# Performance work log

Hardware: AMD Instinct MI355X
Metric: run time of the kernel (lower is better)

## Reference

```python
import jax, jax.numpy as jnp
import numpy as np

OUT_H, OUT_W = 64, 64  # glimpse size (layer's output_dim)
B, IMG_H, IMG_W, CH = 32, 512, 512, 3


def setup_inputs() -> dict:
    key = jax.random.key(0)
    k_img, k_u, k_s, k_d, k_u2, k_s2, k_d2 = jax.random.split(key, 7)
    img_tensor = jax.random.uniform(k_img, (B, IMG_H, IMG_W, CH), dtype=jnp.float32)
    # DRAW-style params per sample: (uy, sy, dy, ux, sx, dx)
    # centres u in [0, img - glimpse], sigma s in [1, 5], stride d in [1, img/glimpse]
    uy = jax.random.uniform(k_u, (B, 1), minval=0.0, maxval=IMG_H - OUT_H * 2.0)
    sy = jax.random.uniform(k_s, (B, 1), minval=1.0, maxval=5.0)
    dy = jax.random.uniform(k_d, (B, 1), minval=1.0, maxval=IMG_H / OUT_H)
    ux = jax.random.uniform(k_u2, (B, 1), minval=0.0, maxval=IMG_W - OUT_W * 2.0)
    sx = jax.random.uniform(k_s2, (B, 1), minval=1.0, maxval=5.0)
    dx = jax.random.uniform(k_d2, (B, 1), minval=1.0, maxval=IMG_W / OUT_W)
    transform_params = jnp.concatenate([uy, sy, dy, ux, sx, dx], axis=-1)  # (B, 6)
    return {"img_tensor": img_tensor, "transform_params": transform_params}


def gaussian_mask(u, s, d, R, C):
    """Normalized Gaussian filterbank.
    u, s, d: (B, 1) centre of first Gaussian, std, stride between centres.
    R: number of glimpse rows/cols; C: image size along that axis.
    Returns (B, C, R), each column normalized to sum 1 (plus eps)."""
    r = jnp.arange(R, dtype=jnp.float32).reshape(1, 1, R)
    c = jnp.arange(C, dtype=jnp.float32).reshape(1, C, 1)
    centres = u[:, None, :] + r * d[:, None, :]            # (B, 1, R)
    mask = jnp.exp(-0.5 * jnp.square((c - centres) / s[:, None, :]))  # (B, C, R)
    return mask / (jnp.sum(mask, axis=1, keepdims=True) + 1e-8)


def reference(img_tensor, transform_params):
    # img_tensor: (B, h, w, ch); transform_params: (B, 6)
    _, h, w, _ = img_tensor.shape
    uy, sy, dy, ux, sx, dx = jnp.split(transform_params, 6, axis=-1)
    Ay = gaussian_mask(uy, sy, dy, OUT_H, h)  # (B, h, OUT_H)
    Ax = gaussian_mask(ux, sx, dx, OUT_W, w)  # (B, w, OUT_W)
    # glimpse = Ay^T @ img @ Ax, applied per channel
    g = jnp.einsum('bhH,bhwc->bHwc', Ay, img_tensor)   # (B, OUT_H, w, ch)
    return jnp.einsum('bHwc,bwW->bHWc', g, Ax)         # (B, OUT_H, OUT_W, ch)
```

## Files before the change

kernel.cpp:

```cpp
#include <hip/hip_runtime.h>
#include <stdint.h>

#define BATCH 32
#define IMG 512
#define CH 3
#define GOUT 64
#define ROWB (IMG*CH)
#define GP   ((size_t)BATCH*CH*GOUT*IMG)

typedef __attribute__((ext_vector_type(8))) short  short8;
typedef __attribute__((ext_vector_type(4))) float  floatx4;

__device__ __forceinline__ unsigned short f2bf(float x) {
    unsigned u = __builtin_bit_cast(unsigned, x);
    u += 0x7FFFu + ((u >> 16) & 1u);
    return (unsigned short)(u >> 16);
}

__global__ __launch_bounds__(64) void mask_kernel(const float* __restrict__ tp,
                                                  unsigned short* __restrict__ AyT,
                                                  unsigned short* __restrict__ AxT) {
    int blk  = blockIdx.x;
    int r    = blk & 63;
    int axis = (blk >> 6) & 1;
    int b    = blk >> 7;

    const float* p = tp + b*6 + (axis ? 3 : 0);
    float u = p[0], s = p[1], d = p[2];
    float centre = u + (float)r * d;
    float inv_s  = 1.0f / s;

    int lane = threadIdx.x;
    float e[8];
    float sum = 0.0f;
    #pragma unroll
    for (int i = 0; i < 8; ++i) {
        float z = ((float)(i*64 + lane) - centre) * inv_s;
        e[i] = __expf(-0.5f * z * z);
        sum += e[i];
    }
    #pragma unroll
    for (int m = 1; m < 64; m <<= 1)
        sum += __shfl_xor(sum, m, 64);
    float inv_sum = 1.0f / (sum + 1e-8f);

    unsigned short* dst = (axis ? AxT : AyT) + ((size_t)b*GOUT + r) * IMG;
    #pragma unroll
    for (int i = 0; i < 8; ++i)
        dst[i*64 + lane] = f2bf(e[i] * inv_sum);
}

__global__ __launch_bounds__(256, 4) void stage1_kernel(const float* __restrict__ img,
                                                        const unsigned short* __restrict__ AyT,
                                                        float* __restrict__ gP) {
    int part = blockIdx.x & 1;
    int bt   = blockIdx.x >> 1;
    int tile = bt % 24;
    int b    = bt / 24;
    int wc0  = tile * 64;
    int tid  = threadIdx.x;
    int wave = tid >> 6;
    int lane = tid & 63;
    int n16  = lane & 15;
    int q    = lane >> 4;

    floatx4 acc[4];
    #pragma unroll
    for (int mt = 0; mt < 4; ++mt) acc[mt] = (floatx4){0.f, 0.f, 0.f, 0.f};

    const float*          imb = img + (size_t)b * IMG * ROWB + wc0 + wave*16 + n16;
    const unsigned short* ayb = AyT + (size_t)b * GOUT * IMG;

    for (int h0 = part*256; h0 < part*256 + 256; h0 += 32) {
        int hk = h0 + q*8;
        const float* ip = imb + (size_t)hk * ROWB;
        short8 bf;
        #pragma unroll
        for (int j = 0; j < 8; ++j)
            bf[j] = (short)f2bf(ip[(size_t)j * ROWB]);
        #pragma unroll
        for (int mt = 0; mt < 4; ++mt) {
            short8 af = *(const short8*)(ayb + (size_t)(mt*16 + n16) * IMG + hk);
            acc[mt] = __builtin_amdgcn_mfma_f32_16x16x32_bf16(af, bf, acc[mt], 0, 0, 0);
        }
    }

    int wc = wc0 + wave*16 + n16;
    int c = wc % 3, w = wc / 3;
    float* gb = gP + (size_t)part * GP + ((size_t)(b*CH + c) * GOUT) * IMG + w;
    #pragma unroll
    for (int mt = 0; mt < 4; ++mt)
        #pragma unroll
        for (int reg = 0; reg < 4; ++reg)
            gb[(size_t)(mt*16 + q*4 + reg) * IMG] = acc[mt][reg];
}

__global__ __launch_bounds__(256) void stage2_kernel(const float* __restrict__ gP,
                                                     const unsigned short* __restrict__ AxT,
                                                     float* __restrict__ out) {
    int blk  = blockIdx.x;
    int hq   = blk & 3;
    int bc   = blk >> 2;
    int c    = bc % 3;
    int b    = bc / 3;
    int tid  = threadIdx.x;
    int wave = tid >> 6;
    int lane = tid & 63;
    int n16  = lane & 15;
    int q    = lane >> 4;

    floatx4 acc = (floatx4){0.f, 0.f, 0.f, 0.f};

    const float*          ga  = gP  + ((size_t)(b*CH + c) * GOUT + hq*16 + n16) * IMG;
    const unsigned short* axb = AxT + ((size_t)b*GOUT + wave*16 + n16) * IMG;

    #pragma unroll 4
    for (int cc = 0; cc < 16; ++cc) {
        int w0 = cc*32 + q*8;
        float4 a0 = *(const float4*)(ga + w0);
        float4 a1 = *(const float4*)(ga + w0 + 4);
        float4 b0 = *(const float4*)(ga + GP + w0);
        float4 b1 = *(const float4*)(ga + GP + w0 + 4);
        short8 af;
        af[0] = (short)f2bf(a0.x + b0.x); af[1] = (short)f2bf(a0.y + b0.y);
        af[2] = (short)f2bf(a0.z + b0.z); af[3] = (short)f2bf(a0.w + b0.w);
        af[4] = (short)f2bf(a1.x + b1.x); af[5] = (short)f2bf(a1.y + b1.y);
        af[6] = (short)f2bf(a1.z + b1.z); af[7] = (short)f2bf(a1.w + b1.w);

        short8 bf = *(const short8*)(axb + w0);
        acc = __builtin_amdgcn_mfma_f32_16x16x32_bf16(af, bf, acc, 0, 0, 0);
    }

    float* ob = out + (((size_t)b*GOUT + hq*16) * GOUT + wave*16 + n16) * CH + c;
    #pragma unroll
    for (int reg = 0; reg < 4; ++reg)
        ob[(size_t)(q*4 + reg) * GOUT * CH] = acc[reg];
}

extern "C" void kernel_launch(void* const* d_in, const int* in_sizes, int n_in,
                              void* d_out, int out_size, void* d_ws, size_t ws_size,
                              hipStream_t stream) {
    const float* img = (const float*)d_in[0];
    const float* tp  = (const float*)d_in[1];
    float* out = (float*)d_out;

    unsigned short* AyT = (unsigned short*)d_ws;
    unsigned short* AxT = AyT + (size_t)BATCH * GOUT * IMG;
    float*          gPp = (float*)(AxT + (size_t)BATCH * GOUT * IMG);

    mask_kernel  <<<BATCH * 2 * GOUT,  64, 0, stream>>>(tp, AyT, AxT);
    stage1_kernel<<<BATCH * 24 * 2,   256, 0, stream>>>(img, AyT, gPp);
    stage2_kernel<<<BATCH * CH * 4,   256, 0, stream>>>(gPp, AxT, out);
}
```

Baseline: 200.2 us.

## Stage image tiles through swizzled LDS with coalesced float4 loads; split stage2 over W

Stage1 now loads the image with coalesced float4 row reads into a 64x64 LDS tile using an XOR swizzle. It register-prefetches the next tile before the MFMA loop and raises the occupancy hint. Before this, each lane did strided scalar loads across rows. Stage2 splits the reduction over W into two halves and accumulates with atomicAdd into an output zeroed by an added memset. This doubles parallelism at the cost of atomics and an extra launch.

Result: faster. 190.0 us (-5.1%).

```diff
diff --git a/kernel.cpp b/kernel.cpp
--- a/kernel.cpp
+++ b/kernel.cpp
@@ -10,6 +10,7 @@
 
 typedef __attribute__((ext_vector_type(8))) short  short8;
 typedef __attribute__((ext_vector_type(4))) float  floatx4;
+typedef __attribute__((ext_vector_type(4))) float  floatv4;
 
 __device__ __forceinline__ unsigned short f2bf(float x) {
     unsigned u = __builtin_bit_cast(unsigned, x);
@@ -50,9 +51,11 @@
         dst[i*64 + lane] = f2bf(e[i] * inv_sum);
 }
 
-__global__ __launch_bounds__(256, 4) void stage1_kernel(const float* __restrict__ img,
+__global__ __launch_bounds__(256, 6) void stage1_kernel(const float* __restrict__ img,
                                                         const unsigned short* __restrict__ AyT,
                                                         float* __restrict__ gP) {
+    __shared__ float Bs[64*64];
+
     int part = blockIdx.x & 1;
     int bt   = blockIdx.x >> 1;
     int tile = bt % 24;
@@ -64,29 +67,71 @@
     int n16  = lane & 15;
     int q    = lane >> 4;
 
+    int hrow = tid >> 4;
+    int col4 = tid & 15;
+
     floatx4 acc[4];
     #pragma unroll
     for (int mt = 0; mt < 4; ++mt) acc[mt] = (floatx4){0.f, 0.f, 0.f, 0.f};
 
-    const float*          imb = img + (size_t)b * IMG * ROWB + wc0 + wave*16 + n16;
+    const float*          imb = img + (size_t)b * IMG * ROWB + wc0 + col4*4;
     const unsigned short* ayb = AyT + (size_t)b * GOUT * IMG;
-
-    for (int h0 = part*256; h0 < part*256 + 256; h0 += 32) {
-        int hk = h0 + q*8;
-        const float* ip = imb + (size_t)hk * ROWB;
-        short8 bf;
+    int h0 = part * 256;
+
+    floatv4 rr[4];
+    #define LOADT(t) do { \
+        const floatv4* p_ = (const floatv4*)(imb + (size_t)(h0 + (t)*64 + hrow) * ROWB); \
+        rr[0] = p_[0]; \
+        rr[1] = p_[(16*ROWB)/4]; \
+        rr[2] = p_[(32*ROWB)/4]; \
+        rr[3] = p_[(48*ROWB)/4]; \
+    } while (0)
+
+    LOADT(0);
+
+    for (int t = 0; t < 4; ++t) {
         #pragma unroll
-        for (int j = 0; j < 8; ++j)
-            bf[j] = (short)f2bf(ip[(size_t)j * ROWB]);
+        for (int r = 0; r < 4; ++r) {
+            int hg = 4*r + (hrow >> 2);
+            int ho = hrow & 3;
+            #pragma unroll
+            for (int i = 0; i < 4; ++i) {
+                int wc = col4*4 + i;
+                Bs[wc*64 + ((hg ^ col4) << 2) + ho] = rr[r][i];
+            }
+        }
+        __syncthreads();
+
+        if (t < 3) LOADT(t+1);
+
+        int hb  = h0 + t*64;
+        int wc  = wave*16 + n16;
+        int key = (wc >> 2);
+        int wcr = wc * 64;
         #pragma unroll
-        for (int mt = 0; mt < 4; ++mt) {
-            short8 af = *(const short8*)(ayb + (size_t)(mt*16 + n16) * IMG + hk);
-            acc[mt] = __builtin_amdgcn_mfma_f32_16x16x32_bf16(af, bf, acc[mt], 0, 0, 0);
+        for (int s = 0; s < 2; ++s) {
+            int hg0 = s*8 + q*2;
+            floatv4 v0 = *(const floatv4*)&Bs[wcr + ((hg0       ^ key) << 2)];
+            floatv4 v1 = *(const floatv4*)&Bs[wcr + (((hg0 + 1) ^ key) << 2)];
+            short8 bf;
+            bf[0] = (short)f2bf(v0[0]); bf[1] = (short)f2bf(v0[1]);
+            bf[2] = (short)f2bf(v0[2]); bf[3] = (short)f2bf(v0[3]);
+            bf[4] = (short)f2bf(v1[0]); bf[5] = (short)f2bf(v1[1]);
+            bf[6] = (short)f2bf(v1[2]); bf[7] = (short)f2bf(v1[3]);
+
+            int hk = hb + s*32 + q*8;
+            #pragma unroll
+            for (int mt = 0; mt < 4; ++mt) {
+                short8 af = *(const short8*)(ayb + (size_t)(mt*16 + n16) * IMG + hk);
+                acc[mt] = __builtin_amdgcn_mfma_f32_16x16x32_bf16(af, bf, acc[mt], 0, 0, 0);
+            }
         }
+        __syncthreads();
     }
-
-    int wc = wc0 + wave*16 + n16;
-    int c = wc % 3, w = wc / 3;
+    #undef LOADT
+
+    int wcg = wc0 + wave*16 + n16;
+    int c = wcg % 3, w = wcg / 3;
     float* gb = gP + (size_t)part * GP + ((size_t)(b*CH + c) * GOUT) * IMG + w;
     #pragma unroll
     for (int mt = 0; mt < 4; ++mt)
@@ -99,8 +144,9 @@
                                                      const unsigned short* __restrict__ AxT,
                                                      float* __restrict__ out) {
     int blk  = blockIdx.x;
-    int hq   = blk & 3;
-    int bc   = blk >> 2;
+    int part = blk & 1;
+    int hq   = (blk >> 1) & 3;
+    int bc   = blk >> 3;
     int c    = bc % 3;
     int b    = bc / 3;
     int tid  = threadIdx.x;
@@ -114,18 +160,18 @@
     const float*          ga  = gP  + ((size_t)(b*CH + c) * GOUT + hq*16 + n16) * IMG;
     const unsigned short* axb = AxT + ((size_t)b*GOUT + wave*16 + n16) * IMG;
 
-    #pragma unroll 4
-    for (int cc = 0; cc < 16; ++cc) {
-        int w0 = cc*32 + q*8;
-        float4 a0 = *(const float4*)(ga + w0);
-        float4 a1 = *(const float4*)(ga + w0 + 4);
-        float4 b0 = *(const float4*)(ga + GP + w0);
-        float4 b1 = *(const float4*)(ga + GP + w0 + 4);
+    #pragma unroll
+    for (int cc = 0; cc < 8; ++cc) {
+        int w0 = part*256 + cc*32 + q*8;
+        floatv4 a0 = *(const floatv4*)(ga + w0);
+        floatv4 a1 = *(const floatv4*)(ga + w0 + 4);
+        floatv4 b0 = *(const floatv4*)(ga + GP + w0);
+        floatv4 b1 = *(const floatv4*)(ga + GP + w0 + 4);
         short8 af;
-        af[0] = (short)f2bf(a0.x + b0.x); af[1] = (short)f2bf(a0.y + b0.y);
-        af[2] = (short)f2bf(a0.z + b0.z); af[3] = (short)f2bf(a0.w + b0.w);
-        af[4] = (short)f2bf(a1.x + b1.x); af[5] = (short)f2bf(a1.y + b1.y);
-        af[6] = (short)f2bf(a1.z + b1.z); af[7] = (short)f2bf(a1.w + b1.w);
+        af[0] = (short)f2bf(a0[0] + b0[0]); af[1] = (short)f2bf(a0[1] + b0[1]);
+        af[2] = (short)f2bf(a0[2] + b0[2]); af[3] = (short)f2bf(a0[3] + b0[3]);
+        af[4] = (short)f2bf(a1[0] + b1[0]); af[5] = (short)f2bf(a1[1] + b1[1]);
+        af[6] = (short)f2bf(a1[2] + b1[2]); af[7] = (short)f2bf(a1[3] + b1[3]);
 
         short8 bf = *(const short8*)(axb + w0);
         acc = __builtin_amdgcn_mfma_f32_16x16x32_bf16(af, bf, acc, 0, 0, 0);
@@ -134,7 +180,7 @@
     float* ob = out + (((size_t)b*GOUT + hq*16) * GOUT + wave*16 + n16) * CH + c;
     #pragma unroll
     for (int reg = 0; reg < 4; ++reg)
-        ob[(size_t)(q*4 + reg) * GOUT * CH] = acc[reg];
+        atomicAdd(ob + (size_t)(q*4 + reg) * GOUT * CH, acc[reg]);
 }
 
 extern "C" void kernel_launch(void* const* d_in, const int* in_sizes, int n_in,
@@ -148,7 +194,8 @@
     unsigned short* AxT = AyT + (size_t)BATCH * GOUT * IMG;
     float*          gPp = (float*)(AxT + (size_t)BATCH * GOUT * IMG);
 
-    mask_kernel  <<<BATCH * 2 * GOUT,  64, 0, stream>>>(tp, AyT, AxT);
-    stage1_kernel<<<BATCH * 24 * 2,   256, 0, stream>>>(img, AyT, gPp);
-    stage2_kernel<<<BATCH * CH * 4,   256, 0, stream>>>(gPp, AxT, out);
-}
+    hipMemsetAsync(d_out, 0, (size_t)out_size * sizeof(float), stream);
+    mask_kernel  <<<BATCH * 2 * GOUT,    64, 0, stream>>>(tp, AyT, AxT);
+    stage1_kernel<<<BATCH * 24 * 2,     256, 0, stream>>>(img, AyT, gPp);
+    stage2_kernel<<<BATCH * CH * 4 * 2, 256, 0, stream>>>(gPp, AxT, out);
+}
```

## Stage image tiles through LDS asynchronously and split stage2 reduction with atomics

Applied to the files above, without the earlier changes.

Stage1 now copies 64x64 float tiles of the image into a double-buffered LDS array with async global-to-LDS loads. The waves then read their bf16 operands from LDS instead of issuing strided per-element global loads, and the next tile's fetch overlaps the current tile's MFMAs. Stage2 splits the w reduction into two halves across twice as many blocks and hoists all loads ahead of the MFMAs. Partial sums are combined with float atomicAdd into an output that a memset zeroes first, which adds a memset launch and atomic traffic and makes the summation order nondeterministic.

Result: faster. 190.6 us (-4.8%).

```diff
diff --git a/kernel.cpp b/kernel.cpp
--- a/kernel.cpp
+++ b/kernel.cpp
@@ -10,11 +10,19 @@
 
 typedef __attribute__((ext_vector_type(8))) short  short8;
 typedef __attribute__((ext_vector_type(4))) float  floatx4;
+typedef __attribute__((ext_vector_type(4))) float  floatv4;
 
 __device__ __forceinline__ unsigned short f2bf(float x) {
     unsigned u = __builtin_bit_cast(unsigned, x);
     u += 0x7FFFu + ((u >> 16) & 1u);
     return (unsigned short)(u >> 16);
+}
+
+typedef __attribute__((address_space(3))) unsigned int  lds_u32;
+typedef __attribute__((address_space(1))) const unsigned int g_u32;
+__device__ __forceinline__ void async16(const void* g, void* l) {
+    __builtin_amdgcn_global_load_lds((g_u32*)(uintptr_t)g,
+                                     (lds_u32*)(uintptr_t)l, 16, 0, 0);
 }
 
 __global__ __launch_bounds__(64) void mask_kernel(const float* __restrict__ tp,
@@ -53,6 +61,8 @@
 __global__ __launch_bounds__(256, 4) void stage1_kernel(const float* __restrict__ img,
                                                         const unsigned short* __restrict__ AyT,
                                                         float* __restrict__ gP) {
+    __shared__ float Bs[2][64][64];
+
     int part = blockIdx.x & 1;
     int bt   = blockIdx.x >> 1;
     int tile = bt % 24;
@@ -68,22 +78,46 @@
     #pragma unroll
     for (int mt = 0; mt < 4; ++mt) acc[mt] = (floatx4){0.f, 0.f, 0.f, 0.f};
 
-    const float*          imb = img + (size_t)b * IMG * ROWB + wc0 + wave*16 + n16;
+    const float*          imb = img + (size_t)b * IMG * ROWB + wc0;
     const unsigned short* ayb = AyT + (size_t)b * GOUT * IMG;
 
-    for (int h0 = part*256; h0 < part*256 + 256; h0 += 32) {
-        int hk = h0 + q*8;
-        const float* ip = imb + (size_t)hk * ROWB;
-        short8 bf;
-        #pragma unroll
-        for (int j = 0; j < 8; ++j)
-            bf[j] = (short)f2bf(ip[(size_t)j * ROWB]);
-        #pragma unroll
-        for (int mt = 0; mt < 4; ++mt) {
-            short8 af = *(const short8*)(ayb + (size_t)(mt*16 + n16) * IMG + hk);
-            acc[mt] = __builtin_amdgcn_mfma_f32_16x16x32_bf16(af, bf, acc[mt], 0, 0, 0);
+    int rb = wave*4 + q;
+    int cg = n16;
+    int h0 = part * 256;
+
+    #define STAGE(t, buf) do { \
+        _Pragma("unroll") \
+        for (int i = 0; i < 4; ++i) { \
+            int r_ = rb + i*16; \
+            async16(imb + (size_t)(h0 + (t)*64 + r_) * ROWB + cg*4, &Bs[buf][r_][cg*4]); \
+        } \
+    } while (0)
+
+    STAGE(0, 0);
+    __syncthreads();
+
+    int cur = 0;
+    for (int t = 0; t < 4; ++t) {
+        if (t < 3) STAGE(t+1, cur ^ 1);
+
+        int hb = h0 + t*64;
+        #pragma unroll
+        for (int s = 0; s < 2; ++s) {
+            short8 bf;
+            #pragma unroll
+            for (int j = 0; j < 8; ++j)
+                bf[j] = (short)f2bf(Bs[cur][s*32 + q*8 + j][wave*16 + n16]);
+            int hk = hb + s*32 + q*8;
+            #pragma unroll
+            for (int mt = 0; mt < 4; ++mt) {
+                short8 af = *(const short8*)(ayb + (size_t)(mt*16 + n16) * IMG + hk);
+                acc[mt] = __builtin_amdgcn_mfma_f32_16x16x32_bf16(af, bf, acc[mt], 0, 0, 0);
+            }
         }
+        __syncthreads();
+        cur ^= 1;
     }
+    #undef STAGE
 
     int wc = wc0 + wave*16 + n16;
     int c = wc % 3, w = wc / 3;
@@ -95,16 +129,17 @@
             gb[(size_t)(mt*16 + q*4 + reg) * IMG] = acc[mt][reg];
 }
 
-__global__ __launch_bounds__(256) void stage2_kernel(const float* __restrict__ gP,
-                                                     const unsigned short* __restrict__ AxT,
-                                                     float* __restrict__ out) {
+__global__ __launch_bounds__(256, 4) void stage2_kernel(const float* __restrict__ gP,
+                                                        const unsigned short* __restrict__ AxT,
+                                                        float* __restrict__ out) {
     int blk  = blockIdx.x;
-    int hq   = blk & 3;
-    int bc   = blk >> 2;
+    int part = blk & 1;
+    int hq   = (blk >> 1) & 3;
+    int bc   = blk >> 3;
     int c    = bc % 3;
     int b    = bc / 3;
     int tid  = threadIdx.x;
-    int wave = tid >> 6;
+    int wq   = tid >> 6;
     int lane = tid & 63;
     int n16  = lane & 15;
     int q    = lane >> 4;
@@ -112,29 +147,40 @@
     floatx4 acc = (floatx4){0.f, 0.f, 0.f, 0.f};
 
     const float*          ga  = gP  + ((size_t)(b*CH + c) * GOUT + hq*16 + n16) * IMG;
-    const unsigned short* axb = AxT + ((size_t)b*GOUT + wave*16 + n16) * IMG;
-
-    #pragma unroll 4
-    for (int cc = 0; cc < 16; ++cc) {
-        int w0 = cc*32 + q*8;
-        float4 a0 = *(const float4*)(ga + w0);
-        float4 a1 = *(const float4*)(ga + w0 + 4);
-        float4 b0 = *(const float4*)(ga + GP + w0);
-        float4 b1 = *(const float4*)(ga + GP + w0 + 4);
-        short8 af;
-        af[0] = (short)f2bf(a0.x + b0.x); af[1] = (short)f2bf(a0.y + b0.y);
-        af[2] = (short)f2bf(a0.z + b0.z); af[3] = (short)f2bf(a0.w + b0.w);
-        af[4] = (short)f2bf(a1.x + b1.x); af[5] = (short)f2bf(a1.y + b1.y);
-        af[6] = (short)f2bf(a1.z + b1.z); af[7] = (short)f2bf(a1.w + b1.w);
-
-        short8 bf = *(const short8*)(axb + w0);
-        acc = __builtin_amdgcn_mfma_f32_16x16x32_bf16(af, bf, acc, 0, 0, 0);
+    const unsigned short* axb = AxT + ((size_t)b*GOUT + wq*16 + n16) * IMG;
+
+    #pragma unroll
+    for (int ph = 0; ph < 2; ++ph) {
+        floatv4 A0[4], A1[4], B0[4], B1[4];
+        short8  BF[4];
+        #pragma unroll
+        for (int cc = 0; cc < 4; ++cc) {
+            int w0 = part*256 + ph*128 + cc*32 + q*8;
+            A0[cc] = *(const floatv4*)(ga + w0);
+            A1[cc] = *(const floatv4*)(ga + w0 + 4);
+            B0[cc] = *(const floatv4*)(ga + GP + w0);
+            B1[cc] = *(const floatv4*)(ga + GP + w0 + 4);
+            BF[cc] = *(const short8*)(axb + w0);
+        }
+        #pragma unroll
+        for (int cc = 0; cc < 4; ++cc) {
+            short8 af;
+            af[0] = (short)f2bf(A0[cc][0] + B0[cc][0]);
+            af[1] = (short)f2bf(A0[cc][1] + B0[cc][1]);
+            af[2] = (short)f2bf(A0[cc][2] + B0[cc][2]);
+            af[3] = (short)f2bf(A0[cc][3] + B0[cc][3]);
+            af[4] = (short)f2bf(A1[cc][0] + B1[cc][0]);
+            af[5] = (short)f2bf(A1[cc][1] + B1[cc][1]);
+            af[6] = (short)f2bf(A1[cc][2] + B1[cc][2]);
+            af[7] = (short)f2bf(A1[cc][3] + B1[cc][3]);
+            acc = __builtin_amdgcn_mfma_f32_16x16x32_bf16(af, BF[cc], acc, 0, 0, 0);
+        }
     }
 
-    float* ob = out + (((size_t)b*GOUT + hq*16) * GOUT + wave*16 + n16) * CH + c;
+    float* ob = out + (((size_t)b*GOUT + hq*16) * GOUT + wq*16 + n16) * CH + c;
     #pragma unroll
     for (int reg = 0; reg < 4; ++reg)
-        ob[(size_t)(q*4 + reg) * GOUT * CH] = acc[reg];
+        atomicAdd(ob + (size_t)(q*4 + reg) * GOUT * CH, acc[reg]);
 }
 
 extern "C" void kernel_launch(void* const* d_in, const int* in_sizes, int n_in,
@@ -148,7 +194,8 @@
     unsigned short* AxT = AyT + (size_t)BATCH * GOUT * IMG;
     float*          gPp = (float*)(AxT + (size_t)BATCH * GOUT * IMG);
 
-    mask_kernel  <<<BATCH * 2 * GOUT,  64, 0, stream>>>(tp, AyT, AxT);
-    stage1_kernel<<<BATCH * 24 * 2,   256, 0, stream>>>(img, AyT, gPp);
-    stage2_kernel<<<BATCH * CH * 4,   256, 0, stream>>>(gPp, AxT, out);
-}
+    hipMemsetAsync(d_out, 0, (size_t)out_size * sizeof(float), stream);
+    mask_kernel  <<<BATCH * 2 * GOUT,    64, 0, stream>>>(tp, AyT, AxT);
+    stage1_kernel<<<BATCH * 24 * 2,     256, 0, stream>>>(img, AyT, gPp);
+    stage2_kernel<<<BATCH * CH * 4 * 2, 256, 0, stream>>>(gPp, AxT, out);
+}
```
